# Performance work log

Measured on AMD Instinct MI355X. Metric: run time of the kernel, lower is better.

Reference implementation:

```python
import jax, jax.numpy as jnp
import numpy as np

# ---- static configuration (mirrors TimeFold init + deterministic prepare()) ----
B = 256
F = 512            # fft_length//2 + 1
T = 81             # input STFT frames
WIN = 1022         # window_length == frame_length == fft_length
HOP = 400          # hop_length
SEG = 1000         # segment_length
OVL = 50           # overlap_length
TO_HOP = 100       # deterministic choice of randint(1, hop_size=100)
SIG_LEN = (T - 1) * HOP + WIN            # 33022, inverse_stft output length

# prepare(): t segments kept, gaps of TO_HOP deleted
_t = SIG_LEN // (SEG + TO_HOP)
if SIG_LEN % (SEG + TO_HOP) >= SEG:
    _t += 1                               # _t = 30
KEPT_LEN = _t * SEG                       # 30000
OUT_LEN = SEG + (_t - 1) * (SEG - OVL)    # 28550
NF = 1 + (OUT_LEN - WIN) // HOP           # 69 output STFT frames

# indices kept after deleting the to_hop gaps (complement of delete_indices)
KEEP_IDX = np.concatenate([k * (SEG + TO_HOP) + np.arange(SEG) for k in range(_t)])

# overlap-add blending coefficients (length KEPT_LEN), built exactly as in prepare()
_ramp_up = np.arange(1, OVL + 1, dtype=np.float32) / OVL
_ramp_dn = np.arange(OVL, 0, -1, dtype=np.float32) / OVL
COEFF_INC = np.pad(np.tile(np.pad(_ramp_up, (0, SEG - OVL)), _t - 1), (SEG - OVL, OVL))
COEFF_DEC = np.pad(np.tile(np.pad(_ramp_dn, (SEG - OVL, 0)), _t - 1), (0, SEG))
_c = np.tile(np.pad(np.ones(SEG - 2 * OVL, np.float32), (OVL, OVL)), _t - 2)
_c = np.pad(np.pad(_c, (OVL, 0)), (SEG - OVL, 0), constant_values=1.0)
_c = np.pad(np.pad(_c, (0, OVL)), (0, SEG - OVL), constant_values=1.0)
COEFF_CONST = _c.astype(np.float32)

# final_delete_indices: drop [k*SEG, k*SEG+OVL) for k = 1.._t-1
_mask = np.ones(KEPT_LEN, bool)
for k in range(1, _t):
    _mask[k * SEG:k * SEG + OVL] = False
FINAL_KEEP = np.nonzero(_mask)[0]         # length OUT_LEN

# gather index grids for framing (static)
ISTFT_IDX = np.arange(T)[:, None] * HOP + np.arange(WIN)[None, :]
STFT_IDX = np.arange(NF)[:, None] * HOP + np.arange(WIN)[None, :]


def _hann(n):
    # periodic Hann, matches tf.signal.hann_window(periodic=True)
    return (0.5 - 0.5 * jnp.cos(2.0 * jnp.pi * jnp.arange(n, dtype=jnp.float32) / n)).astype(jnp.float32)


def _synthesis_window():
    w = _hann(WIN)
    denom = w * w
    overlaps = -(-WIN // HOP)
    denom = jnp.pad(denom, (0, overlaps * HOP - WIN))
    denom = denom.reshape(overlaps, HOP).sum(axis=0)
    denom = jnp.tile(denom, overlaps)[:WIN]
    return w / denom


def setup_inputs() -> dict:
    key = jax.random.key(0)
    x = jax.random.normal(key, (B, F, T, 2), dtype=jnp.float32)
    return {"x": x}


def reference(x) -> jnp.ndarray:
    # x: [B, 512, T, 2] real/imag STFT
    stfts = jax.lax.complex(x[..., 0], x[..., 1])          # [B, F, T]
    frames = jnp.transpose(stfts, (0, 2, 1))               # [B, T, F]
    # inverse_stft: irfft each frame, apply synthesis window, overlap-add
    tf_frames = jnp.fft.irfft(frames, n=WIN, axis=-1)
    tf_frames = tf_frames * _synthesis_window()
    sig = jnp.zeros((x.shape[0], SIG_LEN), jnp.float32).at[:, ISTFT_IDX].add(tf_frames)
    # dynamic segment delete (gather of kept indices)
    kept = sig[:, KEEP_IDX]                                # [B, KEPT_LEN]
    # shifted copy: drop first OVL samples, zero-pad at end
    shifted = jnp.concatenate(
        [kept[:, OVL:], jnp.zeros((x.shape[0], OVL), jnp.float32)], axis=1)
    # weighted overlap-add blend
    out = (jnp.asarray(COEFF_CONST) + jnp.asarray(COEFF_DEC)) * kept \
        + jnp.asarray(COEFF_INC) * shifted
    out = out[:, FINAL_KEEP]                               # [B, OUT_LEN]
    # forward STFT (periodic Hann, no padding)
    fr = out[:, STFT_IDX] * _hann(WIN)
    S = jnp.fft.rfft(fr, n=WIN, axis=-1)                   # [B, NF, 512]
    S = jnp.transpose(S, (0, 2, 1))                        # [B, 512, NF]
    return jnp.stack([S.real, S.imag], axis=-1)            # [B, 512, NF, 2]
```

## Files before the change

### kernel.cpp

```cpp
#include <hip/hip_runtime.h>
#include <math.h>

typedef unsigned short u16;
typedef unsigned int u32;

#define B_   256
#define F_   512
#define T_   81
#define WIN_ 1022
#define HOP_ 400
#define NF_  69
#define OUT_LEN_ 28550
#define SEG_ 1000
#define OVL_ 50

#define MA_  20736
#define MB_  17664
#define K_   1024

#define SYNWIN_B   0u
#define HANN_B     4096u
#define BASA_B     8192u
#define BASB_B     (BASA_B + 2097152u)
#define ABUF_B     (BASB_B + 2097152u)
#define TF_B       (ABUF_B + 42467328u)
#define OUTF_B     (TF_B + 42467328u)
#define OUTF_STRIDE_ 28672
#define FBUF_B     ABUF_B

typedef __attribute__((ext_vector_type(8))) short bf8_t;
typedef __attribute__((ext_vector_type(4))) float f4_t;
typedef const __attribute__((address_space(1))) void* as1cv;
typedef __attribute__((address_space(3))) void* as3v;

__device__ __forceinline__ float b2f(u16 v) {
  u32 u = ((u32)v) << 16; float f; __builtin_memcpy(&f, &u, 4); return f;
}
__device__ __forceinline__ u16 f2b(float f) {
  u32 u; __builtin_memcpy(&u, &f, 4);
  return (u16)((u + 0x7fffu + ((u >> 16) & 1u)) >> 16);
}

__global__ __launch_bounds__(256) void k1_tables(float* __restrict__ ws) {
  int i = blockIdx.x * 256 + threadIdx.x;
  if (i >= WIN_) return;
  const float twopi_N = 6.283185307179586f / (float)WIN_;
  float w = 0.5f - 0.5f * cosf(twopi_N * (float)i);
  int j = i % HOP_;
  float a = 0.5f - 0.5f * cosf(twopi_N * (float)j);
  float b = 0.5f - 0.5f * cosf(twopi_N * (float)(j + 400));
  float d = a * a + b * b;
  if (j + 800 < WIN_) {
    float c = 0.5f - 0.5f * cosf(twopi_N * (float)(j + 800));
    d += c * c;
  }
  ((float*)((char*)ws + SYNWIN_B))[i] = w / d;
  ((float*)((char*)ws + HANN_B))[i]   = w;
}

__global__ __launch_bounds__(256) void gen_basisA(const float* __restrict__ synwin,
                                                  u16* __restrict__ BA) {
  int n = blockIdx.x;
  float scale = (n < WIN_) ? synwin[n] * (1.0f / (float)WIN_) : 0.f;
  for (int k = threadIdx.x; k < 512; k += 256) {
    int m = (k * n) % WIN_;
    float ang = 6.283185307179586f * (float)m / (float)WIN_;
    float s, c; __sincosf(ang, &s, &c);
    bool edge = (k == 0) || (k == 511);
    float ck = edge ? 1.f : 2.f;
    float re = scale * ck * c;
    float im = edge ? 0.f : -scale * ck * s;
    BA[(size_t)n * K_ + 2 * k]     = f2b(re);
    BA[(size_t)n * K_ + 2 * k + 1] = f2b(im);
  }
}

__global__ __launch_bounds__(256) void gen_basisB(u16* __restrict__ BB) {
  int k = blockIdx.x;
  for (int w = threadIdx.x; w < K_; w += 256) {
    float re = 0.f, im = 0.f;
    if (w < WIN_) {
      int m = (k * w) % WIN_;
      float ang = 6.283185307179586f * (float)m / (float)WIN_;
      float s, c; __sincosf(ang, &s, &c);
      re = c; im = -s;
    }
    BB[(size_t)(2 * k)     * K_ + w] = f2b(re);
    BB[(size_t)(2 * k + 1) * K_ + w] = f2b(im);
  }
}

__global__ __launch_bounds__(256) void prep1(const float* __restrict__ x,
                                             u16* __restrict__ Abuf) {
  __shared__ float2 tile[32][33];
  int k0 = blockIdx.x * 32, t0 = blockIdx.y * 32, b = blockIdx.z;
  int c = threadIdx.x & 31, rr = threadIdx.x >> 5;
  const float2* xp = (const float2*)x;
#pragma unroll
  for (int i = 0; i < 4; ++i) {
    int k = k0 + rr + 8 * i, t = t0 + c;
    float2 v = make_float2(0.f, 0.f);
    if (t < T_) v = xp[(size_t)(b * F_ + k) * T_ + t];
    tile[rr + 8 * i][c] = v;
  }
  __syncthreads();
#pragma unroll
  for (int i = 0; i < 4; ++i) {
    int t = t0 + rr + 8 * i, kc = c;
    if (t < T_) {
      float2 v = tile[kc][rr + 8 * i];
      u32 packed = (u32)f2b(v.x) | ((u32)f2b(v.y) << 16);
      *(u32*)&Abuf[(size_t)(b * T_ + t) * K_ + 2 * (k0 + kc)] = packed;
    }
  }
}

template <int EPI>
__global__ __launch_bounds__(256) void gemm_bf16(const u16* __restrict__ A,
                                                 const u16* __restrict__ Bt,
                                                 void* __restrict__ Cout) {
  __shared__ u16 sA[128 * 32];
  __shared__ u16 sB[128 * 32];
  const int tid = threadIdx.x;
  const int lane = tid & 63, wv = tid >> 6;
  const int bm = blockIdx.x * 128, bn = blockIdx.y * 128;

  const int c0 = wv * 2;
  const int srow = 16 * c0 + (lane >> 2);
  const int scol = (lane & 3) * 8;
  const u16* gA0 = A  + (size_t)(bm + srow) * K_ + scol;
  const u16* gA1 = gA0 + (size_t)16 * K_;
  const u16* gB0 = Bt + (size_t)(bn + srow) * K_ + scol;
  const u16* gB1 = gB0 + (size_t)16 * K_;
  u16* lA0 = sA + c0 * 512;
  u16* lA1 = lA0 + 512;
  u16* lB0 = sB + c0 * 512;
  u16* lB1 = lB0 + 512;

  f4_t acc[4][4];
#pragma unroll
  for (int i = 0; i < 4; ++i)
#pragma unroll
    for (int j = 0; j < 4; ++j) acc[i][j] = (f4_t){0.f, 0.f, 0.f, 0.f};

  const int wm = (wv >> 1) * 64, wn = (wv & 1) * 64;
  const int frow = lane & 15;
  const int fcol = (lane >> 4) * 8;

  for (int k0 = 0; k0 < K_; k0 += 32) {
    __builtin_amdgcn_global_load_lds((as1cv)(const void*)(gA0 + k0), (as3v)lA0, 16, 0, 0);
    __builtin_amdgcn_global_load_lds((as1cv)(const void*)(gA1 + k0), (as3v)lA1, 16, 0, 0);
    __builtin_amdgcn_global_load_lds((as1cv)(const void*)(gB0 + k0), (as3v)lB0, 16, 0, 0);
    __builtin_amdgcn_global_load_lds((as1cv)(const void*)(gB1 + k0), (as3v)lB1, 16, 0, 0);
    __builtin_amdgcn_s_waitcnt(0x0f70);
    __syncthreads();

    bf8_t af[4], bq[4];
#pragma unroll
    for (int i = 0; i < 4; ++i)
      af[i] = *(const bf8_t*)&sA[(wm + 16 * i + frow) * 32 + fcol];
#pragma unroll
    for (int j = 0; j < 4; ++j)
      bq[j] = *(const bf8_t*)&sB[(wn + 16 * j + frow) * 32 + fcol];
#pragma unroll
    for (int i = 0; i < 4; ++i)
#pragma unroll
      for (int j = 0; j < 4; ++j)
        acc[i][j] = __builtin_amdgcn_mfma_f32_16x16x32_bf16(af[i], bq[j], acc[i][j], 0, 0, 0);
    __syncthreads();
  }

  if (EPI == 0) {
    u16* C = (u16*)Cout;
#pragma unroll
    for (int i = 0; i < 4; ++i)
#pragma unroll
      for (int j = 0; j < 4; ++j) {
        int colg = bn + wn + 16 * j + frow;
#pragma unroll
        for (int r = 0; r < 4; ++r) {
          int rowg = bm + wm + 16 * i + (lane >> 4) * 4 + r;
          C[(size_t)rowg * K_ + colg] = f2b(acc[i][j][r]);
        }
      }
  } else {
    float* out = (float*)Cout;
    float* ep = ((wv & 2) ? (float*)sB : (float*)sA) + (wv & 1) * 1024;
    for (int j = 0; j < 4; ++j) {
#pragma unroll
      for (int i = 0; i < 4; ++i)
#pragma unroll
        for (int r = 0; r < 4; ++r) {
          int row64 = 16 * i + (lane >> 4) * 4 + r;
          ep[row64 * 16 + frow] = acc[i][j][r];
        }
      __syncthreads();
      int m = bm + wm + lane;
      int b = m / NF_;
      int f = m - b * NF_;
      int colbase = bn + wn + 16 * j;
#pragma unroll
      for (int a = 0; a < 8; ++a) {
        int k = (colbase >> 1) + a;
        float2 v = make_float2(ep[lane * 16 + 2 * a], ep[lane * 16 + 2 * a + 1]);
        ((float2*)out)[((size_t)b * F_ + k) * NF_ + f] = v;
      }
      __syncthreads();
    }
  }
}

__device__ __forceinline__ float sigval(const u16* __restrict__ tfb, int i) {
  int t1 = i / HOP_; if (t1 > T_ - 1) t1 = T_ - 1;
  int t0 = (i >= WIN_) ? (i - (WIN_ - 1) + HOP_ - 1) / HOP_ : 0;
  float acc = 0.f;
  for (int t = t0; t <= t1; ++t)
    acc += b2f(tfb[(size_t)t * K_ + (i - t * HOP_)]);
  return acc;
}

__global__ __launch_bounds__(256) void k3_fold(const u16* __restrict__ tf,
                                               u16* __restrict__ outf) {
  int id = blockIdx.x * 256 + threadIdx.x;
  if (id >= B_ * OUT_LEN_) return;
  int b = id / OUT_LEN_;
  int p = id - b * OUT_LEN_;
  int s, r;
  if (p < SEG_) { s = 0; r = p; }
  else {
    int q = p - SEG_;
    s = q / (SEG_ - OVL_) + 1;
    r = OVL_ + (q - (s - 1) * (SEG_ - OVL_));
  }
  const u16* tfb = tf + (size_t)b * T_ * K_;
  float val;
  if (r >= SEG_ - OVL_ && s <= 28) {
    float dec = (float)(SEG_ - r) * (1.f / (float)OVL_);
    float inc = (float)(r - (SEG_ - OVL_ - 1)) * (1.f / (float)OVL_);
    float v1 = sigval(tfb, s * 1100 + r);
    float v2 = sigval(tfb, (s + 1) * 1100 + (r - (SEG_ - OVL_)));
    val = dec * v1 + inc * v2;
  } else {
    val = sigval(tfb, s * 1100 + r);
  }
  outf[(size_t)b * OUTF_STRIDE_ + p] = f2b(val);
}

__global__ __launch_bounds__(256) void prep2(const u16* __restrict__ outf,
                                             const float* __restrict__ hann,
                                             u16* __restrict__ Fbuf) {
  int bf = blockIdx.x;
  int b = bf / NF_, f = bf - b * NF_;
  int w0 = threadIdx.x * 4;
  const u16* src = outf + (size_t)b * OUTF_STRIDE_ + f * HOP_ + w0;
  ushort4 in = *(const ushort4*)src;
  u16 o[4];
  float vv[4] = {b2f(in.x), b2f(in.y), b2f(in.z), b2f(in.w)};
#pragma unroll
  for (int ii = 0; ii < 4; ++ii) {
    int w = w0 + ii;
    o[ii] = (w < WIN_) ? f2b(vv[ii] * hann[w]) : (u16)0;
  }
  *(ushort4*)&Fbuf[(size_t)bf * K_ + w0] = make_ushort4(o[0], o[1], o[2], o[3]);
}

extern "C" void kernel_launch(void* const* d_in, const int* in_sizes, int n_in,
                              void* d_out, int out_size, void* d_ws, size_t ws_size,
                              hipStream_t stream) {
  const float* x = (const float*)d_in[0];
  char* ws = (char*)d_ws;
  float* synwin = (float*)(ws + SYNWIN_B);
  float* hann   = (float*)(ws + HANN_B);
  u16* BA   = (u16*)(ws + BASA_B);
  u16* BB   = (u16*)(ws + BASB_B);
  u16* Abuf = (u16*)(ws + ABUF_B);
  u16* TF   = (u16*)(ws + TF_B);
  u16* outf = (u16*)(ws + OUTF_B);
  u16* Fbuf = (u16*)(ws + FBUF_B);
  float* out = (float*)d_out;

  hipLaunchKernelGGL(k1_tables, dim3(4), dim3(256), 0, stream, (float*)ws);
  hipLaunchKernelGGL(gen_basisA, dim3(1024), dim3(256), 0, stream, synwin, BA);
  hipLaunchKernelGGL(gen_basisB, dim3(512), dim3(256), 0, stream, BB);
  hipLaunchKernelGGL(prep1, dim3(16, 3, 256), dim3(256), 0, stream, x, Abuf);
  hipLaunchKernelGGL((gemm_bf16<0>), dim3(MA_ / 128, 8), dim3(256), 0, stream,
                     Abuf, BA, (void*)TF);
  int n3 = B_ * OUT_LEN_;
  hipLaunchKernelGGL(k3_fold, dim3((n3 + 255) / 256), dim3(256), 0, stream, TF, outf);
  hipLaunchKernelGGL(prep2, dim3(MB_), dim3(256), 0, stream, outf, hann, Fbuf);
  hipLaunchKernelGGL((gemm_bf16<1>), dim3(MB_ / 128, 8), dim3(256), 0, stream,
                     Fbuf, BB, (void*)d_out);
}
```

Baseline: 352.9 us.

## Fold Hann window into DFT basis and gather STFT frames directly in GEMM

Multiplies the Hann window into the forward DFT basis and removes the prep2 framing kernel. The second GEMM now loads overlapping frames directly from the folded signal buffer via per-row offsets. Both GEMMs also switch to a 1D grid with an XCD-aware tile mapping and a fragment-major LDS layout. This saves one kernel launch and a full write/read of the frame buffer. The cost is strided, overlapping A-row loads and padded grid blocks that exit early.

```diff
diff --git a/kernel.cpp b/kernel.cpp
--- a/kernel.cpp
+++ b/kernel.cpp
@@ -17,6 +17,10 @@
 #define MA_  20736
 #define MB_  17664
 #define K_   1024
+#define NMA_TILES 162
+#define NMB_TILES 138
+#define NMA_PAD   168
+#define NMB_PAD   144
 
 #define SYNWIN_B   0u
 #define HANN_B     4096u
@@ -26,7 +30,6 @@
 #define TF_B       (ABUF_B + 42467328u)
 #define OUTF_B     (TF_B + 42467328u)
 #define OUTF_STRIDE_ 28672
-#define FBUF_B     ABUF_B
 
 typedef __attribute__((ext_vector_type(8))) short bf8_t;
 typedef __attribute__((ext_vector_type(4))) float f4_t;
@@ -75,7 +78,8 @@
   }
 }
 
-__global__ __launch_bounds__(256) void gen_basisB(u16* __restrict__ BB) {
+__global__ __launch_bounds__(256) void gen_basisB(const float* __restrict__ hann,
+                                                  u16* __restrict__ BB) {
   int k = blockIdx.x;
   for (int w = threadIdx.x; w < K_; w += 256) {
     float re = 0.f, im = 0.f;
@@ -83,7 +87,8 @@
       int m = (k * w) % WIN_;
       float ang = 6.283185307179586f * (float)m / (float)WIN_;
       float s, c; __sincosf(ang, &s, &c);
-      re = c; im = -s;
+      float h = hann[w];
+      re = h * c; im = -h * s;
     }
     BB[(size_t)(2 * k)     * K_ + w] = f2b(re);
     BB[(size_t)(2 * k + 1) * K_ + w] = f2b(im);
@@ -119,23 +124,41 @@
 __global__ __launch_bounds__(256) void gemm_bf16(const u16* __restrict__ A,
                                                  const u16* __restrict__ Bt,
                                                  void* __restrict__ Cout) {
-  __shared__ u16 sA[128 * 32];
-  __shared__ u16 sB[128 * 32];
+  __shared__ u16 sA[8 * 512];
+  __shared__ u16 sB[8 * 512];
   const int tid = threadIdx.x;
   const int lane = tid & 63, wv = tid >> 6;
-  const int bm = blockIdx.x * 128, bn = blockIdx.y * 128;
-
-  const int c0 = wv * 2;
-  const int srow = 16 * c0 + (lane >> 2);
-  const int scol = (lane & 3) * 8;
-  const u16* gA0 = A  + (size_t)(bm + srow) * K_ + scol;
-  const u16* gA1 = gA0 + (size_t)16 * K_;
-  const u16* gB0 = Bt + (size_t)(bn + srow) * K_ + scol;
-  const u16* gB1 = gB0 + (size_t)16 * K_;
-  u16* lA0 = sA + c0 * 512;
-  u16* lA1 = lA0 + 512;
-  u16* lB0 = sB + c0 * 512;
-  u16* lB1 = lB0 + 512;
+
+  int id = blockIdx.x;
+  int xcd = id & 7, slot = id >> 3;
+  int mt = (slot >> 3) * 8 + xcd;
+  int nt = slot & 7;
+  const int nM = (EPI == 0) ? NMA_TILES : NMB_TILES;
+  if (mt >= nM) return;
+  const int bm = mt * 128, bn = nt * 128;
+
+  const int fr = lane & 15, fq = lane >> 4;
+  const int s0 = 2 * wv, s1 = s0 + 1;
+
+  const u16 *pA0, *pA1;
+  if (EPI == 0) {
+    pA0 = A + (size_t)(bm + 16 * s0 + fr) * K_ + fq * 8;
+    pA1 = A + (size_t)(bm + 16 * s1 + fr) * K_ + fq * 8;
+  } else {
+    int m0 = bm + 16 * s0 + fr;
+    int b0 = m0 / NF_, f0 = m0 - b0 * NF_;
+    pA0 = A + (size_t)b0 * OUTF_STRIDE_ + f0 * HOP_ + fq * 8;
+    int m1 = m0 + 16;
+    int b1 = m1 / NF_, f1 = m1 - b1 * NF_;
+    pA1 = A + (size_t)b1 * OUTF_STRIDE_ + f1 * HOP_ + fq * 8;
+  }
+  const u16* pB0 = Bt + (size_t)(bn + 16 * s0 + fr) * K_ + fq * 8;
+  const u16* pB1 = Bt + (size_t)(bn + 16 * s1 + fr) * K_ + fq * 8;
+
+  u16* lA0 = sA + s0 * 512;
+  u16* lA1 = sA + s1 * 512;
+  u16* lB0 = sB + s0 * 512;
+  u16* lB1 = sB + s1 * 512;
 
   f4_t acc[4][4];
 #pragma unroll
@@ -143,25 +166,23 @@
 #pragma unroll
     for (int j = 0; j < 4; ++j) acc[i][j] = (f4_t){0.f, 0.f, 0.f, 0.f};
 
-  const int wm = (wv >> 1) * 64, wn = (wv & 1) * 64;
-  const int frow = lane & 15;
-  const int fcol = (lane >> 4) * 8;
+  const int wm4 = (wv >> 1) * 4, wn4 = (wv & 1) * 4;
 
   for (int k0 = 0; k0 < K_; k0 += 32) {
-    __builtin_amdgcn_global_load_lds((as1cv)(const void*)(gA0 + k0), (as3v)lA0, 16, 0, 0);
-    __builtin_amdgcn_global_load_lds((as1cv)(const void*)(gA1 + k0), (as3v)lA1, 16, 0, 0);
-    __builtin_amdgcn_global_load_lds((as1cv)(const void*)(gB0 + k0), (as3v)lB0, 16, 0, 0);
-    __builtin_amdgcn_global_load_lds((as1cv)(const void*)(gB1 + k0), (as3v)lB1, 16, 0, 0);
+    __builtin_amdgcn_global_load_lds((as1cv)(const void*)(pA0 + k0), (as3v)lA0, 16, 0, 0);
+    __builtin_amdgcn_global_load_lds((as1cv)(const void*)(pA1 + k0), (as3v)lA1, 16, 0, 0);
+    __builtin_amdgcn_global_load_lds((as1cv)(const void*)(pB0 + k0), (as3v)lB0, 16, 0, 0);
+    __builtin_amdgcn_global_load_lds((as1cv)(const void*)(pB1 + k0), (as3v)lB1, 16, 0, 0);
     __builtin_amdgcn_s_waitcnt(0x0f70);
     __syncthreads();
 
     bf8_t af[4], bq[4];
 #pragma unroll
     for (int i = 0; i < 4; ++i)
-      af[i] = *(const bf8_t*)&sA[(wm + 16 * i + frow) * 32 + fcol];
+      af[i] = *(const bf8_t*)&sA[(wm4 + i) * 512 + lane * 8];
 #pragma unroll
     for (int j = 0; j < 4; ++j)
-      bq[j] = *(const bf8_t*)&sB[(wn + 16 * j + frow) * 32 + fcol];
+      bq[j] = *(const bf8_t*)&sB[(wn4 + j) * 512 + lane * 8];
 #pragma unroll
     for (int i = 0; i < 4; ++i)
 #pragma unroll
@@ -170,16 +191,17 @@
     __syncthreads();
   }
 
+  const int wm = wm4 * 16, wn = wn4 * 16;
   if (EPI == 0) {
     u16* C = (u16*)Cout;
 #pragma unroll
     for (int i = 0; i < 4; ++i)
 #pragma unroll
       for (int j = 0; j < 4; ++j) {
-        int colg = bn + wn + 16 * j + frow;
+        int colg = bn + wn + 16 * j + fr;
 #pragma unroll
         for (int r = 0; r < 4; ++r) {
-          int rowg = bm + wm + 16 * i + (lane >> 4) * 4 + r;
+          int rowg = bm + wm + 16 * i + fq * 4 + r;
           C[(size_t)rowg * K_ + colg] = f2b(acc[i][j][r]);
         }
       }
@@ -191,8 +213,8 @@
       for (int i = 0; i < 4; ++i)
 #pragma unroll
         for (int r = 0; r < 4; ++r) {
-          int row64 = 16 * i + (lane >> 4) * 4 + r;
-          ep[row64 * 16 + frow] = acc[i][j][r];
+          int row64 = 16 * i + fq * 4 + r;
+          ep[row64 * 16 + fr] = acc[i][j][r];
         }
       __syncthreads();
       int m = bm + wm + lane;
@@ -246,24 +268,6 @@
   outf[(size_t)b * OUTF_STRIDE_ + p] = f2b(val);
 }
 
-__global__ __launch_bounds__(256) void prep2(const u16* __restrict__ outf,
-                                             const float* __restrict__ hann,
-                                             u16* __restrict__ Fbuf) {
-  int bf = blockIdx.x;
-  int b = bf / NF_, f = bf - b * NF_;
-  int w0 = threadIdx.x * 4;
-  const u16* src = outf + (size_t)b * OUTF_STRIDE_ + f * HOP_ + w0;
-  ushort4 in = *(const ushort4*)src;
-  u16 o[4];
-  float vv[4] = {b2f(in.x), b2f(in.y), b2f(in.z), b2f(in.w)};
-#pragma unroll
-  for (int ii = 0; ii < 4; ++ii) {
-    int w = w0 + ii;
-    o[ii] = (w < WIN_) ? f2b(vv[ii] * hann[w]) : (u16)0;
-  }
-  *(ushort4*)&Fbuf[(size_t)bf * K_ + w0] = make_ushort4(o[0], o[1], o[2], o[3]);
-}
-
 extern "C" void kernel_launch(void* const* d_in, const int* in_sizes, int n_in,
                               void* d_out, int out_size, void* d_ws, size_t ws_size,
                               hipStream_t stream) {
@@ -276,18 +280,15 @@
   u16* Abuf = (u16*)(ws + ABUF_B);
   u16* TF   = (u16*)(ws + TF_B);
   u16* outf = (u16*)(ws + OUTF_B);
-  u16* Fbuf = (u16*)(ws + FBUF_B);
-  float* out = (float*)d_out;
 
   hipLaunchKernelGGL(k1_tables, dim3(4), dim3(256), 0, stream, (float*)ws);
   hipLaunchKernelGGL(gen_basisA, dim3(1024), dim3(256), 0, stream, synwin, BA);
-  hipLaunchKernelGGL(gen_basisB, dim3(512), dim3(256), 0, stream, BB);
+  hipLaunchKernelGGL(gen_basisB, dim3(512), dim3(256), 0, stream, hann, BB);
   hipLaunchKernelGGL(prep1, dim3(16, 3, 256), dim3(256), 0, stream, x, Abuf);
-  hipLaunchKernelGGL((gemm_bf16<0>), dim3(MA_ / 128, 8), dim3(256), 0, stream,
+  hipLaunchKernelGGL((gemm_bf16<0>), dim3(NMA_PAD * 8), dim3(256), 0, stream,
                      Abuf, BA, (void*)TF);
   int n3 = B_ * OUT_LEN_;
   hipLaunchKernelGGL(k3_fold, dim3((n3 + 255) / 256), dim3(256), 0, stream, TF, outf);
-  hipLaunchKernelGGL(prep2, dim3(MB_), dim3(256), 0, stream, outf, hann, Fbuf);
-  hipLaunchKernelGGL((gemm_bf16<1>), dim3(MB_ / 128, 8), dim3(256), 0, stream,
-                     Fbuf, BB, (void*)d_out);
-}
+  hipLaunchKernelGGL((gemm_bf16<1>), dim3(NMB_PAD * 8), dim3(256), 0, stream,
+                     outf, BB, (void*)d_out);
+}
```

Measured after the change: 364.3 us. 1.03x slower.
